# Performance work log

Measured on AMD Instinct MI355X. Metric: run time of the kernel, lower is better.

The kernel has to match this reference:

```python
import jax, jax.numpy as jnp
import numpy as np

B, T, NF, D = 32, 128, 20, 512
S = 5            # num_sample
L = 96           # seq_len per utterance (static)
EPS = 1e-8


def _cosine(a, b):
    # torch.F.cosine_similarity: dot / max(|a|*|b|, eps)
    num = jnp.sum(a * b, axis=-1)
    den = jnp.maximum(
        jnp.sqrt(jnp.sum(a * a, axis=-1)) * jnp.sqrt(jnp.sum(b * b, axis=-1)), EPS
    )
    return num / den


def setup_inputs() -> dict:
    key = jax.random.key(0)
    output = jax.random.normal(key, (B, T, NF, D), dtype=jnp.float32)

    # static segment gather indices: seq_len = L for every utterance
    batch_idx = jnp.asarray(np.repeat(np.arange(B), L), dtype=jnp.int32)
    time_idx = jnp.asarray(np.tile(np.arange(L), B), dtype=jnp.int32)

    # negative frame indices: for anchor frame i, sample S frames from
    # {0..NF-1} \ {i-1, i, i+1} (matches masked randperm sampling)
    rng = np.random.default_rng(0)
    neg = np.empty((NF - 1, S), dtype=np.int32)
    all_f = np.arange(NF)
    for i in range(NF - 1):
        allowed = all_f[(all_f != i - 1) & (all_f != i) & (all_f != i + 1)]
        neg[i] = rng.permutation(allowed)[:S]
    neg_idx = jnp.asarray(neg.reshape(-1), dtype=jnp.int32)  # [(NF-1)*S]

    return {"output": output, "batch_idx": batch_idx, "time_idx": time_idx,
            "neg_idx": neg_idx}


def reference(output, batch_idx, time_idx, neg_idx):
    # gather valid segments: [num_seg, NF, D]
    seg = output[batch_idx, time_idx]

    anchors = seg[:, :-1, :]                      # [num_seg, NF-1, D]
    sim_pos = _cosine(anchors, seg[:, 1:, :])     # [num_seg, NF-1]

    # negatives[seg, i, s] = seg[seg, neg_idx[i*S+s]]
    negs = seg[:, neg_idx, :].reshape(seg.shape[0], NF - 1, S, D)
    sim_neg = _cosine(anchors[:, :, None, :], negs)          # [num_seg, NF-1, S]

    sim_all = jnp.concatenate([sim_pos[..., None], sim_neg], axis=-1)
    loss = jnp.mean(-jax.nn.log_softmax(sim_all, axis=-1)[..., 0])
    return loss
```

## Files before the change

kernel.cpp:

```cpp
#include <hip/hip_runtime.h>
#include <hip/hip_bf16.h>
#include <math.h>

#define B_  32
#define T_  128
#define NF_ 20
#define D_  512
#define S_  5
#define L_  96
#define EPS_ 1e-8f
#define NSEG (B_ * L_)
#define NPOS (NF_ - 1)
#define NNEG ((NF_ - 1) * S_)
#define NPAIR (NF_ + NPOS + NNEG)
#define NELEM (NF_ * D_)

__global__ __launch_bounds__(256) void phoneme_ssl_loss_kernel(
    const float* __restrict__ out,
    const int* __restrict__ batch_idx,
    const int* __restrict__ time_idx,
    const int* __restrict__ neg_idx,
    float* __restrict__ loss_out) {

  __shared__ float seg[NELEM];
  __shared__ float dots[NPAIR];

  const int n = blockIdx.x;
  const int b = batch_idx[n];
  const int t = time_idx[n];
  const float* __restrict__ src = out + (size_t)(b * T_ + t) * NELEM;

  const float4* __restrict__ src4 = (const float4*)src;
  float4* seg4 = (float4*)seg;
#pragma unroll
  for (int i = 0; i < NELEM / 4 / 256; ++i)
    seg4[threadIdx.x + 256 * i] = src4[threadIdx.x + 256 * i];
  __syncthreads();

  const int wave = threadIdx.x >> 6;
  const int lane = threadIdx.x & 63;
  for (int p = wave; p < NPAIR; p += 4) {
    int fa, fb;
    if (p < NF_) {
      fa = p; fb = p;
    } else if (p < NF_ + NPOS) {
      fa = p - NF_; fb = fa + 1;
    } else {
      int q = p - NF_ - NPOS;
      fa = q / S_;
      fb = neg_idx[q];
    }
    const float* __restrict__ va = seg + fa * D_;
    const float* __restrict__ vb = seg + fb * D_;
    float acc = 0.f;
#pragma unroll
    for (int k = 0; k < D_ / 64; ++k)
      acc += va[lane + 64 * k] * vb[lane + 64 * k];
#pragma unroll
    for (int off = 32; off >= 1; off >>= 1)
      acc += __shfl_xor(acc, off, 64);
    if (lane == 0) dots[p] = acc;
  }
  __syncthreads();

  float local = 0.f;
  if (threadIdx.x < NPOS) {
    const int i = threadIdx.x;
    const float na = sqrtf(dots[i]);
    float sims[1 + S_];
    {
      const float nb = sqrtf(dots[i + 1]);
      sims[0] = dots[NF_ + i] / fmaxf(na * nb, EPS_);
    }
#pragma unroll
    for (int j = 0; j < S_; ++j) {
      const int fb = neg_idx[i * S_ + j];
      const float nb = sqrtf(dots[fb]);
      sims[1 + j] = dots[NF_ + NPOS + i * S_ + j] / fmaxf(na * nb, EPS_);
    }
    float m = sims[0];
#pragma unroll
    for (int j = 1; j < 1 + S_; ++j) m = fmaxf(m, sims[j]);
    float se = 0.f;
#pragma unroll
    for (int j = 0; j < 1 + S_; ++j) se += __expf(sims[j] - m);
    const float lse = m + __logf(se);
    local = -(sims[0] - lse);
  }

  if (threadIdx.x < 64) {
#pragma unroll
    for (int off = 32; off >= 1; off >>= 1)
      local += __shfl_xor(local, off, 64);
    if (threadIdx.x == 0)
      atomicAdd(loss_out, local * (1.0f / (float)(NSEG * NPOS)));
  }
}

extern "C" void kernel_launch(void* const* d_in, const int* in_sizes, int n_in,
                              void* d_out, int out_size, void* d_ws, size_t ws_size,
                              hipStream_t stream) {
  const float* out_t    = (const float*)d_in[0];
  const int* batch_idx  = (const int*)d_in[1];
  const int* time_idx   = (const int*)d_in[2];
  const int* neg_idx    = (const int*)d_in[3];
  float* loss_out       = (float*)d_out;

  hipMemsetAsync(loss_out, 0, sizeof(float), stream);

  phoneme_ssl_loss_kernel<<<NSEG, 256, 0, stream>>>(
      out_t, batch_idx, time_idx, neg_idx, loss_out);
}
```

Measured before the change: 273.4 us.

## Compute per-segment Gram matrix with bf16 MFMA instead of scalar dot products

Each segment's frames are converted to bf16 in shared memory, and one wave computes the full 20x20 Gram matrix with 16x16x32 bf16 MFMA instructions. The per-pair wave-reduction dot products are removed, and cosine similarities are then read from the Gram matrix. This cuts LDS traffic and shuffle reductions, but bf16 rounding lowers precision, and only one wave of four does the matrix work. The kernel is likely bound by HBM loads of 40KB per segment, so compute savings may matter less.

```diff
diff --git a/kernel.cpp b/kernel.cpp
--- a/kernel.cpp
+++ b/kernel.cpp
@@ -11,9 +11,18 @@
 #define EPS_ 1e-8f
 #define NSEG (B_ * L_)
 #define NPOS (NF_ - 1)
-#define NNEG ((NF_ - 1) * S_)
-#define NPAIR (NF_ + NPOS + NNEG)
 #define NELEM (NF_ * D_)
+#define RPAD (D_ + 8)
+#define GLD 33
+
+typedef short short8 __attribute__((ext_vector_type(8)));
+typedef float f32x4  __attribute__((ext_vector_type(4)));
+
+__device__ __forceinline__ unsigned short f2bf(float f) {
+  unsigned int u = __float_as_uint(f);
+  u += 0x7fffu + ((u >> 16) & 1u);
+  return (unsigned short)(u >> 16);
+}
 
 __global__ __launch_bounds__(256) void phoneme_ssl_loss_kernel(
     const float* __restrict__ out,
@@ -22,8 +31,8 @@
     const int* __restrict__ neg_idx,
     float* __restrict__ loss_out) {
 
-  __shared__ float seg[NELEM];
-  __shared__ float dots[NPAIR];
+  __shared__ __align__(16) unsigned short V[NF_ * RPAD];
+  __shared__ float G[32 * GLD];
 
   const int n = blockIdx.x;
   const int b = batch_idx[n];
@@ -31,60 +40,72 @@
   const float* __restrict__ src = out + (size_t)(b * T_ + t) * NELEM;
 
   const float4* __restrict__ src4 = (const float4*)src;
-  float4* seg4 = (float4*)seg;
 #pragma unroll
-  for (int i = 0; i < NELEM / 4 / 256; ++i)
-    seg4[threadIdx.x + 256 * i] = src4[threadIdx.x + 256 * i];
+  for (int it = 0; it < 5; ++it) {
+    const int c = threadIdx.x + 256 * it;
+    const float4 x = src4[2 * c];
+    const float4 y = src4[2 * c + 1];
+    short8 v;
+    v[0] = (short)f2bf(x.x); v[1] = (short)f2bf(x.y);
+    v[2] = (short)f2bf(x.z); v[3] = (short)f2bf(x.w);
+    v[4] = (short)f2bf(y.x); v[5] = (short)f2bf(y.y);
+    v[6] = (short)f2bf(y.z); v[7] = (short)f2bf(y.w);
+    const int row = c >> 6;
+    const int col = (c & 63) * 8;
+    *(short8*)&V[row * RPAD + col] = v;
+  }
   __syncthreads();
 
-  const int wave = threadIdx.x >> 6;
-  const int lane = threadIdx.x & 63;
-  for (int p = wave; p < NPAIR; p += 4) {
-    int fa, fb;
-    if (p < NF_) {
-      fa = p; fb = p;
-    } else if (p < NF_ + NPOS) {
-      fa = p - NF_; fb = fa + 1;
-    } else {
-      int q = p - NF_ - NPOS;
-      fa = q / S_;
-      fb = neg_idx[q];
+  if (threadIdx.x < 64) {
+    const int lane = threadIdx.x;
+    const int r = lane & 15;
+    const int q = lane >> 4;
+    const int row1 = (16 + r > 19) ? 19 : 16 + r;
+    const unsigned short* p0 = &V[r    * RPAD + q * 8];
+    const unsigned short* p1 = &V[row1 * RPAD + q * 8];
+    f32x4 c00 = {0.f, 0.f, 0.f, 0.f}, c01 = c00, c10 = c00, c11 = c00;
+#pragma unroll
+    for (int ks = 0; ks < D_ / 32; ++ks) {
+      const short8 a0 = *(const short8*)(p0 + 32 * ks);
+      const short8 a1 = *(const short8*)(p1 + 32 * ks);
+      c00 = __builtin_amdgcn_mfma_f32_16x16x32_bf16(a0, a0, c00, 0, 0, 0);
+      c01 = __builtin_amdgcn_mfma_f32_16x16x32_bf16(a0, a1, c01, 0, 0, 0);
+      c10 = __builtin_amdgcn_mfma_f32_16x16x32_bf16(a1, a0, c10, 0, 0, 0);
+      c11 = __builtin_amdgcn_mfma_f32_16x16x32_bf16(a1, a1, c11, 0, 0, 0);
     }
-    const float* __restrict__ va = seg + fa * D_;
-    const float* __restrict__ vb = seg + fb * D_;
-    float acc = 0.f;
 #pragma unroll
-    for (int k = 0; k < D_ / 64; ++k)
-      acc += va[lane + 64 * k] * vb[lane + 64 * k];
-#pragma unroll
-    for (int off = 32; off >= 1; off >>= 1)
-      acc += __shfl_xor(acc, off, 64);
-    if (lane == 0) dots[p] = acc;
+    for (int reg = 0; reg < 4; ++reg) {
+      const int rr = q * 4 + reg;
+      G[rr        * GLD + r]      = c00[reg];
+      G[rr        * GLD + 16 + r] = c01[reg];
+      G[(16 + rr) * GLD + r]      = c10[reg];
+      G[(16 + rr) * GLD + 16 + r] = c11[reg];
+    }
   }
   __syncthreads();
 
   float local = 0.f;
   if (threadIdx.x < NPOS) {
     const int i = threadIdx.x;
-    const float na = sqrtf(dots[i]);
+    const float na = sqrtf(G[i * GLD + i]);
     float sims[1 + S_];
     {
-      const float nb = sqrtf(dots[i + 1]);
-      sims[0] = dots[NF_ + i] / fmaxf(na * nb, EPS_);
+      const float nb = sqrtf(G[(i + 1) * GLD + (i + 1)]);
+      sims[0] = G[i * GLD + (i + 1)] / fmaxf(na * nb, EPS_);
     }
 #pragma unroll
     for (int j = 0; j < S_; ++j) {
-      const int fb = neg_idx[i * S_ + j];
-      const float nb = sqrtf(dots[fb]);
-      sims[1 + j] = dots[NF_ + NPOS + i * S_ + j] / fmaxf(na * nb, EPS_);
+      const int f = neg_idx[i * S_ + j];
+      const float nb = sqrtf(G[f * GLD + f]);
+      sims[1 + j] = G[i * GLD + f] / fmaxf(na * nb, EPS_);
     }
     float m = sims[0];
 #pragma unroll
     for (int j = 1; j < 1 + S_; ++j) m = fmaxf(m, sims[j]);
     float se = 0.f;
 #pragma unroll
-    for (int j = 0; j < 1 + S_; ++j) se += __expf(sims[j] - m);
-    const float lse = m + __logf(se);
+    for (int j = 0; j < 1 + S_; ++j) se += expf(sims[j] - m);
+    const float lse = m + logf(se);
     local = -(sims[0] - lse);
   }
 
```

After: 234.4 us. 14.3% less time.
